# Kernel tuning notes

Hardware: AMD Instinct MI355X
Metric: run time of the kernel (lower is better)

The kernel has to match this reference:

```python
import jax, jax.numpy as jnp
import numpy as np

SMOOTHING = 0.1
CONFIDENCE = 1.0 - SMOOTHING
EPS = 1e-8  # torch CosineSimilarity eps


def setup_inputs() -> dict:
    key = jax.random.key(0)
    k1, k2, k3 = jax.random.split(key, 3)
    B, C, D = 16384, 4096, 1024
    pred = jax.random.normal(k1, (B, C), dtype=jnp.float32)
    weight = jax.random.normal(k2, (C, D), dtype=jnp.float32)
    target = jax.random.randint(k3, (B,), 0, C, dtype=jnp.int64)
    return {"pred": pred, "weight": weight, "target": target}


def _make_confusion(weight):
    # cosine similarity between all pairs of classifier rows (T=1)
    norm = jnp.maximum(jnp.linalg.norm(weight, axis=1, keepdims=True), EPS)
    wn = weight / norm                      # [C, D]
    sim = wn @ wn.T                         # [C, C], diag == 1 (== T)
    e = jnp.exp(sim)
    diag = jnp.diagonal(e)[:, None]
    conf = e / (jnp.sum(e, axis=1, keepdims=True) - diag)
    C = weight.shape[0]
    idx = jnp.arange(C)
    return conf.at[idx, idx].set(0.0)       # zero diagonal after normalization


def reference(pred, weight, target):
    B, C = pred.shape
    logp = jax.nn.log_softmax(pred, axis=-1)          # [B, C]

    confusion = _make_confusion(weight)               # [C, C]
    alpha = confusion[target]                         # [B, C] Dirichlet concentrations (0 at target col)

    # Dirichlet sample via normalized gammas; alpha==0 entries yield exactly 0
    pos = alpha > 0
    g = jax.random.gamma(jax.random.key(42), jnp.where(pos, alpha, 1.0))
    g = jnp.where(pos, g, 0.0)                        # [B, C]
    diri = g / jnp.sum(g, axis=-1, keepdims=True)

    true_dist = diri * SMOOTHING
    true_dist = true_dist.at[jnp.arange(B), target].set(CONFIDENCE)
    true_dist = jax.lax.stop_gradient(true_dist)      # built under no_grad in original

    return jnp.mean(jnp.sum(-true_dist * logp, axis=-1))
```

## Files before the change

kernel.cpp:

```cpp
#include <hip/hip_runtime.h>
#include <hip/hip_bf16.h>

#define CDIM 4096
#define DDIM 1024
#define BDIM 16384
#define EDIAG 2.7182818284590452f
#define QBASE 0.36787944f
#define QSCALE 0.15669957f
#define QINV 6.3816357f

using frag_ab = __attribute__((ext_vector_type(8))) short;
using frag_cd = __attribute__((ext_vector_type(4))) float;
using f32x4   = __attribute__((ext_vector_type(4))) float;

typedef __attribute__((address_space(1))) const void gvoid;
typedef __attribute__((address_space(3))) void lvoid;

__device__ __forceinline__ float block_sum(float v, float* red) {
  int t = threadIdx.x;
  #pragma unroll
  for (int off = 32; off; off >>= 1) v += __shfl_xor(v, off);
  __syncthreads();
  if ((t & 63) == 0) red[t >> 6] = v;
  __syncthreads();
  return (red[0] + red[1]) + (red[2] + red[3]);
}

__device__ __forceinline__ unsigned short f2bfbits(float f) {
  __hip_bfloat16 b = __float2bfloat16(f);
  return *(unsigned short*)&b;
}

__device__ __forceinline__ int q4(float ex) {
  int q = __float2int_rn((ex - QBASE) * QINV);
  return min(15, max(0, q));
}

__global__ __launch_bounds__(256) void k_norm(const float* __restrict__ w,
                                              __hip_bfloat16* __restrict__ wnb,
                                              float* __restrict__ Sf) {
  __shared__ float red[4];
  __shared__ float s_inv;
  int row = blockIdx.x, t = threadIdx.x;
  const float4* wr = (const float4*)(w + (size_t)row * DDIM);
  float4 x = wr[t];
  float ss = (x.x * x.x + x.y * x.y) + (x.z * x.z + x.w * x.w);
  ss = block_sum(ss, red);
  if (t == 0) {
    s_inv = 1.0f / fmaxf(sqrtf(ss), 1e-8f);
    Sf[row] = 0.0f;
  }
  __syncthreads();
  float inv = s_inv;
  ushort4 o;
  o.x = f2bfbits(x.x * inv);
  o.y = f2bfbits(x.y * inv);
  o.z = f2bfbits(x.z * inv);
  o.w = f2bfbits(x.w * inv);
  *(ushort4*)(wnb + (size_t)row * DDIM + t * 4) = o;
}

__global__ __launch_bounds__(512) void k_simexp(const __hip_bfloat16* __restrict__ wb,
                                                unsigned char* __restrict__ e4,
                                                float* __restrict__ Sf) {
  __shared__ char smem[65536];
  int tid = threadIdx.x;
  int lane = tid & 63, wid = tid >> 6;
  int l15 = lane & 15, lk = (lane >> 4) * 8;
  int wm = wid >> 2, wn4 = wid & 3;

  int bi = blockIdx.x;
  int r = (int)((65.0f - sqrtf(4225.0f - 8.0f * (float)bi)) * 0.5f);
  if (r < 0) r = 0; if (r > 31) r = 31;
  while (r * (65 - r) / 2 > bi) --r;
  while ((r + 1) * (64 - r) / 2 <= bi) ++r;
  int brow = r;
  int bcol = r + (bi - r * (65 - r) / 2);
  bool diag = (brow == bcol);

  int srow = tid >> 3;
  int swzel = ((tid & 7) ^ (srow & 7)) * 8;
  const __hip_bfloat16* gA0 = wb + (size_t)(brow * 128 + srow) * DDIM + swzel;
  const __hip_bfloat16* gA1 = gA0 + (size_t)64 * DDIM;
  const __hip_bfloat16* gB0 = wb + (size_t)(bcol * 128 + srow) * DDIM + swzel;
  const __hip_bfloat16* gB1 = gB0 + (size_t)64 * DDIM;
  int ldst = tid * 16;

#define STAGE(bufbase, k0)                                                                  \
  do {                                                                                      \
    __builtin_amdgcn_global_load_lds((gvoid*)(gA0 + (k0)), (lvoid*)(smem + (bufbase) + ldst),         16, 0, 0); \
    __builtin_amdgcn_global_load_lds((gvoid*)(gA1 + (k0)), (lvoid*)(smem + (bufbase) + 8192 + ldst),  16, 0, 0); \
    __builtin_amdgcn_global_load_lds((gvoid*)(gB0 + (k0)), (lvoid*)(smem + (bufbase) + 16384 + ldst), 16, 0, 0); \
    __builtin_amdgcn_global_load_lds((gvoid*)(gB1 + (k0)), (lvoid*)(smem + (bufbase) + 24576 + ldst), 16, 0, 0); \
  } while (0)

  int xorb = (l15 & 7) << 4;
  int aoff = (wm * 64 + l15) * 128;
  int boff = 16384 + (wn4 * 32 + l15) * 128;

  frag_cd acc[4][2] = {};

  STAGE(0, 0);
  int cur = 0;
  for (int t = 0; t < 16; t++) {
    if (t < 15) {
      STAGE((cur ^ 1) * 32768, (t + 1) * 64);
      asm volatile("s_waitcnt vmcnt(4)" ::: "memory");
    } else {
      asm volatile("s_waitcnt vmcnt(0)" ::: "memory");
    }
    __builtin_amdgcn_sched_barrier(0);
    __builtin_amdgcn_s_barrier();
    __builtin_amdgcn_sched_barrier(0);

    const char* base = smem + cur * 32768;
    const char* pa0 = base + aoff;
    const char* pb0 = base + boff;
    #pragma unroll
    for (int ks = 0; ks < 2; ks++) {
      int off = ((ks * 32 + lk) * 2) ^ xorb;
      frag_ab a[4], b[2];
      #pragma unroll
      for (int m = 0; m < 4; m++) a[m] = *(const frag_ab*)(const void*)(pa0 + m * 2048 + off);
      #pragma unroll
      for (int n = 0; n < 2; n++) b[n] = *(const frag_ab*)(const void*)(pb0 + n * 2048 + off);
      #pragma unroll
      for (int m = 0; m < 4; m++)
        #pragma unroll
        for (int n = 0; n < 2; n++)
          acc[m][n] = __builtin_amdgcn_mfma_f32_16x16x32_bf16(a[m], b[n], acc[m][n], 0, 0, 0);
    }

    __builtin_amdgcn_sched_barrier(0);
    __builtin_amdgcn_s_barrier();
    __builtin_amdgcn_sched_barrier(0);
    cur ^= 1;
  }
#undef STAGE

  #pragma unroll
  for (int m = 0; m < 4; m++)
    #pragma unroll
    for (int n = 0; n < 2; n++)
      #pragma unroll
      for (int j = 0; j < 4; j++)
        acc[m][n][j] = __expf(acc[m][n][j]);

  int rg = (lane >> 4) * 4;
  int r0g = brow * 128 + wm * 64;
  int c0g = bcol * 128 + wn4 * 32 + l15;

  #pragma unroll
  for (int m = 0; m < 4; m++)
    #pragma unroll
    for (int j = 0; j < 4; j++) {
      int rglob = r0g + m * 16 + rg + j;
      float rsum = 0.f;
      #pragma unroll
      for (int n = 0; n < 2; n++) {
        float ex = acc[m][n][j];
        rsum += ex;
        int q = q4(ex);
        int qr = __shfl_xor(q, 1);
        if (!(l15 & 1))
          e4[(size_t)rglob * 2048 + (unsigned)((c0g + n * 16) >> 1)] =
              (unsigned char)(q | (qr << 4));
      }
      rsum += __shfl_xor(rsum, 1);
      rsum += __shfl_xor(rsum, 2);
      rsum += __shfl_xor(rsum, 4);
      rsum += __shfl_xor(rsum, 8);
      if (l15 == 0) atomicAdd(&Sf[rglob], rsum);
    }

  if (!diag) {
    #pragma unroll
    for (int n = 0; n < 2; n++) {
      int cg = c0g + n * 16;
      #pragma unroll
      for (int m = 0; m < 4; m++) {
        int b0 = q4(acc[m][n][0]) | (q4(acc[m][n][1]) << 4);
        int b1 = q4(acc[m][n][2]) | (q4(acc[m][n][3]) << 4);
        *(unsigned short*)(e4 + (size_t)cg * 2048 + ((unsigned)(r0g + m * 16 + rg) >> 1)) =
            (unsigned short)(b0 | (b1 << 8));
      }
      float cs = 0.f;
      #pragma unroll
      for (int mm = 0; mm < 4; mm++)
        #pragma unroll
        for (int j = 0; j < 4; j++) cs += acc[mm][n][j];
      cs += __shfl_xor(cs, 16);
      cs += __shfl_xor(cs, 32);
      if (lane < 16) atomicAdd(&Sf[cg], cs);
    }
  }
}

__global__ __launch_bounds__(256) void k_loss(const float* __restrict__ pred,
                                              const int* __restrict__ tgt,
                                              const unsigned char* __restrict__ e4,
                                              const float* __restrict__ Sf,
                                              float* __restrict__ part) {
  __shared__ float reds[4], redq[4], redp[4];
  int i = blockIdx.x, t = threadIdx.x;
  int tg = tgt[i];
  const f32x4* pr = (const f32x4*)(pred + (size_t)i * CDIM);
  const unsigned short* er = (const unsigned short*)(e4 + (size_t)tg * 2048);

  float se = 0.f, sp = 0.f, qd = 0.f;
  #pragma unroll
  for (int j = 0; j < 4; j++) {
    f32x4 v = __builtin_nontemporal_load(pr + t + j * 256);
    unsigned int u = er[t + j * 256];
    se += (__expf(v[0]) + __expf(v[1])) + (__expf(v[2]) + __expf(v[3]));
    sp += (v[0] + v[1]) + (v[2] + v[3]);
    qd += (float)(u & 15u) * v[0] +
          (float)((u >> 4) & 15u) * v[1] +
          (float)((u >> 8) & 15u) * v[2] +
          (float)(u >> 12) * v[3];
  }
  #pragma unroll
  for (int off = 32; off; off >>= 1) {
    se += __shfl_xor(se, off);
    sp += __shfl_xor(sp, off);
    qd += __shfl_xor(qd, off);
  }
  if ((t & 63) == 0) { reds[t >> 6] = se; redq[t >> 6] = qd; redp[t >> 6] = sp; }
  __syncthreads();
  if (t == 0) {
    se = (reds[0] + reds[1]) + (reds[2] + reds[3]);
    qd = (redq[0] + redq[1]) + (redq[2] + redq[3]);
    sp = (redp[0] + redp[1]) + (redp[2] + redp[3]);
    float dot = QSCALE * qd + QBASE * sp;
    float lse = __logf(se);
    float pt = pred[(size_t)i * CDIM + tg];
    float ce = lse - pt;
    float S = Sf[tg];
    float t2 = (S * lse - dot - EDIAG * ce) / (S - EDIAG);
    part[i] = 0.9f * ce + 0.1f * t2;
  }
}

__global__ __launch_bounds__(256) void k_final(const float* __restrict__ part,
                                               float* __restrict__ out) {
  __shared__ float red[4];
  int t = threadIdx.x;
  float s = 0.f;
  for (int i = t; i < BDIM; i += 256) s += part[i];
  s = block_sum(s, red);
  if (t == 0) out[0] = s * (1.0f / BDIM);
}

extern "C" void kernel_launch(void* const* d_in, const int* in_sizes, int n_in,
                              void* d_out, int out_size, void* d_ws, size_t ws_size,
                              hipStream_t stream) {
  const float* pred = (const float*)d_in[0];
  const float* weight = (const float*)d_in[1];
  const int* target = (const int*)d_in[2];
  float* out = (float*)d_out;
  char* ws = (char*)d_ws;

  __hip_bfloat16* wnb = (__hip_bfloat16*)ws;
  unsigned char* e4 = (unsigned char*)(ws + (size_t)(8u << 20));
  float* Sf   = (float*)(ws + (size_t)(16u << 20));
  float* part = (float*)(ws + (size_t)(16u << 20) + 16384);

  k_norm<<<dim3(CDIM), dim3(256), 0, stream>>>(weight, wnb, Sf);
  k_simexp<<<dim3(528), dim3(512), 0, stream>>>(wnb, e4, Sf);
  k_loss<<<dim3(BDIM), dim3(256), 0, stream>>>(pred, target, e4, Sf, part);
  k_final<<<dim3(1), dim3(256), 0, stream>>>(part, out);
}
```

Baseline: 116.2 us.

## Process eight rows per loss block with LDS double-buffered confusion-row prefetch

The loss kernel now launches 2048 persistent-style blocks, each handling eight batch rows. The packed confusion row for the next row's target is prefetched into a double-buffered LDS slot with async global-to-LDS loads while the current row is reduced. The aim is to hide e4 gather latency and cut block launch overhead. In exchange, the extra vmcnt wait and barrier per row serialise the iterations, and fewer blocks may lower the memory parallelism available for streaming pred.

Result: slower. 119.6 us (+2.9%).

```diff
diff --git a/kernel.cpp b/kernel.cpp
--- a/kernel.cpp
+++ b/kernel.cpp
@@ -201,43 +201,64 @@
                                               const unsigned char* __restrict__ e4,
                                               const float* __restrict__ Sf,
                                               float* __restrict__ part) {
-  __shared__ float reds[4], redq[4], redp[4];
-  int i = blockIdx.x, t = threadIdx.x;
-  int tg = tgt[i];
-  const f32x4* pr = (const f32x4*)(pred + (size_t)i * CDIM);
-  const unsigned short* er = (const unsigned short*)(e4 + (size_t)tg * 2048);
-
-  float se = 0.f, sp = 0.f, qd = 0.f;
-  #pragma unroll
-  for (int j = 0; j < 4; j++) {
-    f32x4 v = __builtin_nontemporal_load(pr + t + j * 256);
-    unsigned int u = er[t + j * 256];
-    se += (__expf(v[0]) + __expf(v[1])) + (__expf(v[2]) + __expf(v[3]));
-    sp += (v[0] + v[1]) + (v[2] + v[3]);
-    qd += (float)(u & 15u) * v[0] +
-          (float)((u >> 4) & 15u) * v[1] +
-          (float)((u >> 8) & 15u) * v[2] +
-          (float)(u >> 12) * v[3];
-  }
-  #pragma unroll
-  for (int off = 32; off; off >>= 1) {
-    se += __shfl_xor(se, off);
-    sp += __shfl_xor(sp, off);
-    qd += __shfl_xor(qd, off);
-  }
-  if ((t & 63) == 0) { reds[t >> 6] = se; redq[t >> 6] = qd; redp[t >> 6] = sp; }
-  __syncthreads();
-  if (t == 0) {
-    se = (reds[0] + reds[1]) + (reds[2] + reds[3]);
-    qd = (redq[0] + redq[1]) + (redq[2] + redq[3]);
-    sp = (redp[0] + redp[1]) + (redp[2] + redp[3]);
-    float dot = QSCALE * qd + QBASE * sp;
-    float lse = __logf(se);
-    float pt = pred[(size_t)i * CDIM + tg];
-    float ce = lse - pt;
-    float S = Sf[tg];
-    float t2 = (S * lse - dot - EDIAG * ce) / (S - EDIAG);
-    part[i] = 0.9f * ce + 0.1f * t2;
+  __shared__ uint2 erow[2][256];
+  __shared__ float reds[2][4], redq[2][4], redp[2][4];
+  int b = blockIdx.x, t = threadIdx.x;
+
+  int tgs[8];
+  #pragma unroll
+  for (int s = 0; s < 8; s++) tgs[s] = tgt[s * 2048 + b];
+
+  erow[0][t] = ((const uint2*)(e4 + (size_t)tgs[0] * 2048))[t];
+  __syncthreads();
+
+  #pragma unroll
+  for (int s = 0; s < 8; s++) {
+    int i = s * 2048 + b;
+    int tg = tgs[s];
+    if (s < 7 && t < 128)
+      __builtin_amdgcn_global_load_lds(
+          (gvoid*)(e4 + (size_t)tgs[s + 1] * 2048 + t * 16),
+          (lvoid*)((char*)erow[(s + 1) & 1] + t * 16), 16, 0, 0);
+
+    const f32x4* pr = (const f32x4*)(pred + (size_t)i * CDIM);
+    const unsigned short* er = (const unsigned short*)erow[s & 1];
+
+    float se = 0.f, sp = 0.f, qd = 0.f;
+    #pragma unroll
+    for (int j = 0; j < 4; j++) {
+      f32x4 v = __builtin_nontemporal_load(pr + t + j * 256);
+      unsigned int u = er[t + j * 256];
+      se += (__expf(v[0]) + __expf(v[1])) + (__expf(v[2]) + __expf(v[3]));
+      sp += (v[0] + v[1]) + (v[2] + v[3]);
+      qd += (float)(u & 15u) * v[0] +
+            (float)((u >> 4) & 15u) * v[1] +
+            (float)((u >> 8) & 15u) * v[2] +
+            (float)(u >> 12) * v[3];
+    }
+    #pragma unroll
+    for (int off = 32; off; off >>= 1) {
+      se += __shfl_xor(se, off);
+      sp += __shfl_xor(sp, off);
+      qd += __shfl_xor(qd, off);
+    }
+    if ((t & 63) == 0) {
+      reds[s & 1][t >> 6] = se; redq[s & 1][t >> 6] = qd; redp[s & 1][t >> 6] = sp;
+    }
+    asm volatile("s_waitcnt vmcnt(0)" ::: "memory");
+    __syncthreads();
+    if (t == 0) {
+      float seb = (reds[s & 1][0] + reds[s & 1][1]) + (reds[s & 1][2] + reds[s & 1][3]);
+      float qdb = (redq[s & 1][0] + redq[s & 1][1]) + (redq[s & 1][2] + redq[s & 1][3]);
+      float spb = (redp[s & 1][0] + redp[s & 1][1]) + (redp[s & 1][2] + redp[s & 1][3]);
+      float dot = QSCALE * qdb + QBASE * spb;
+      float lse = __logf(seb);
+      float pt = pred[(size_t)i * CDIM + tg];
+      float ce = lse - pt;
+      float S = Sf[tg];
+      float t2 = (S * lse - dot - EDIAG * ce) / (S - EDIAG);
+      part[i] = 0.9f * ce + 0.1f * t2;
+    }
   }
 }
 
@@ -267,6 +288,6 @@
 
   k_norm<<<dim3(CDIM), dim3(256), 0, stream>>>(weight, wnb, Sf);
   k_simexp<<<dim3(528), dim3(512), 0, stream>>>(wnb, e4, Sf);
-  k_loss<<<dim3(BDIM), dim3(256), 0, stream>>>(pred, target, e4, Sf, part);
+  k_loss<<<dim3(2048), dim3(256), 0, stream>>>(pred, target, e4, Sf, part);
   k_final<<<dim3(1), dim3(256), 0, stream>>>(part, out);
 }
```
